# Kernel tuning notes

Hardware: AMD Instinct MI355X
Metric: run time of the kernel (lower is better)

Reference implementation:

```python
import jax, jax.numpy as jnp
import numpy as np

N_NODES = 100000
N_EDGES = 1600000
IN_SIZE = 128
HIDDEN = 128
OUT_SIZE = 64


def setup_inputs() -> dict:
    key = jax.random.key(0)
    k = jax.random.split(key, 8)
    feat = jax.random.normal(k[0], (N_NODES, IN_SIZE), dtype=jnp.float32)
    src = jax.random.randint(k[1], (N_EDGES,), 0, N_NODES, dtype=jnp.int32)
    dst = jax.random.randint(k[2], (N_EDGES,), 0, N_NODES, dtype=jnp.int32)
    # fc_neigh weights for the two SAGEConv layers (stored as [in, out])
    W1 = jax.random.normal(k[3], (IN_SIZE, HIDDEN), dtype=jnp.float32) / np.sqrt(IN_SIZE)
    b1 = jnp.zeros((HIDDEN,), dtype=jnp.float32)
    W2 = jax.random.normal(k[4], (HIDDEN, OUT_SIZE), dtype=jnp.float32) / np.sqrt(HIDDEN)
    b2 = jnp.zeros((OUT_SIZE,), dtype=jnp.float32)
    return {"feat": feat, "W1": W1, "b1": b1, "W2": W2, "b2": b2,
            "src": src, "dst": dst}


def _sage_gcn(h, src, dst, W, b):
    # DGL SAGEConv with aggregator_type='gcn':
    #   neigh = segment_sum over incoming edges of src features
    #   h_neigh = (neigh + h_self) / (in_degree + 1)
    #   out = h_neigh @ W + b   (fc_self is not used for 'gcn')
    neigh = jax.ops.segment_sum(h[src], dst, num_segments=N_NODES)  # [N, d]
    deg = jax.ops.segment_sum(jnp.ones((src.shape[0],), dtype=h.dtype), dst,
                              num_segments=N_NODES)                 # [N]
    h_neigh = (neigh + h) / (deg + 1.0)[:, None]
    return h_neigh @ W + b


def reference(feat, W1, b1, W2, b2, src, dst):
    # dropout(p=0.0) is identity; activation between layers only
    h = _sage_gcn(feat, src, dst, W1, b1)
    h = jax.nn.relu(h)
    h = _sage_gcn(h, src, dst, W2, b2)
    return h
```

## Files before the change

kernel.cpp:

```cpp
#include <hip/hip_runtime.h>

#define NNODES 100000
#define NEDGES 1600000
#define BSHIFT 7
#define NB 782
#define CAP 2560
#define EBLOCKS 391
#define GEMM_BLOCKS 1563

typedef _Float16 f16;
typedef _Float16 v8h __attribute__((ext_vector_type(8)));
typedef float v4f __attribute__((ext_vector_type(4)));

__device__ inline void acc8(float s, uint2 u, float* a) {
    a[0] = fmaf(s, (float)(u.x & 0xFF), a[0]);
    a[1] = fmaf(s, (float)((u.x >> 8) & 0xFF), a[1]);
    a[2] = fmaf(s, (float)((u.x >> 16) & 0xFF), a[2]);
    a[3] = fmaf(s, (float)(u.x >> 24), a[3]);
    a[4] = fmaf(s, (float)(u.y & 0xFF), a[4]);
    a[5] = fmaf(s, (float)((u.y >> 8) & 0xFF), a[5]);
    a[6] = fmaf(s, (float)((u.y >> 16) & 0xFF), a[6]);
    a[7] = fmaf(s, (float)(u.y >> 24), a[7]);
}

__global__ __launch_bounds__(256) void init_k(int* __restrict__ bcur,
                                              const float* __restrict__ W1,
                                              f16* __restrict__ W1t,
                                              const float* __restrict__ W2,
                                              f16* __restrict__ W2t) {
    int t = blockIdx.x * 256 + threadIdx.x;
    if (t < NB) bcur[t] = t * CAP;
    int u = t - 1024;
    if (u >= 0) {
        if (u < 128 * 128) {
            int k = u >> 7, n = u & 127;
            W1t[n * 128 + k] = (f16)W1[k * 128 + n];
        } else if (u < 128 * 128 + 128 * 64) {
            int v = u - 128 * 128;
            int k = v >> 6, n = v & 63;
            W2t[n * 128 + k] = (f16)W2[k * 64 + n];
        }
    }
}

__global__ __launch_bounds__(256) void scatter_gemm1(
    const int* __restrict__ src, const int* __restrict__ dst,
    int* __restrict__ bcur, int* __restrict__ ebuf,
    const float* __restrict__ feat, const f16* __restrict__ W1t,
    unsigned char* __restrict__ z1, float* __restrict__ sc1) {
    constexpr int PITCH = 136;
    __shared__ __align__(16) char smem[128 * PITCH * 2];
    int tid = threadIdx.x;

    if (blockIdx.x < EBLOCKS) {
        int* h = (int*)smem;
        int* base_s = ((int*)smem) + 1024;
        for (int i = tid; i < NB; i += 256) h[i] = 0;
        __syncthreads();
        int base = blockIdx.x * 4096;
        int d[16], sv[16];
        for (int k = 0; k < 16; k++) {
            int e = base + k * 256 + tid;
            if (e < NEDGES) {
                d[k] = dst[e];
                sv[k] = src[e];
                atomicAdd(&h[d[k] >> BSHIFT], 1);
            } else {
                d[k] = -1;
            }
        }
        __syncthreads();
        for (int i = tid; i < NB; i += 256) {
            int c = h[i];
            if (c) base_s[i] = atomicAdd(&bcur[i], c);
            h[i] = 0;
        }
        __syncthreads();
        for (int k = 0; k < 16; k++) {
            if (d[k] >= 0) {
                int b = d[k] >> BSHIFT;
                int slot = atomicAdd(&h[b], 1);
                ebuf[base_s[b] + slot] = sv[k] | ((d[k] & 127) << 24);
            }
        }
        return;
    }

    f16* wlds = (f16*)smem;
    for (int c = tid; c < 128 * 16; c += 256) {
        int n = c >> 4;
        int kc = c & 15;
        *(v8h*)&wlds[n * PITCH + kc * 8] = *(const v8h*)&W1t[n * 128 + kc * 8];
    }
    __syncthreads();

    int wave = tid >> 6, lane = tid & 63, quad = lane >> 4, l16 = lane & 15;
    int m0 = (blockIdx.x - EBLOCKS) * 64 + wave * 16;
    if (m0 >= NNODES) return;

    v8h a[4];
    const float* arow = feat + (long)(m0 + l16) * 128 + quad * 8;
#pragma unroll
    for (int kb = 0; kb < 4; kb++) {
        float4 f0 = *(const float4*)(arow + kb * 32);
        float4 f1 = *(const float4*)(arow + kb * 32 + 4);
        v8h t = {(f16)f0.x, (f16)f0.y, (f16)f0.z, (f16)f0.w,
                 (f16)f1.x, (f16)f1.y, (f16)f1.z, (f16)f1.w};
        a[kb] = t;
    }

    v4f acc[8];
#pragma unroll
    for (int nt = 0; nt < 8; nt++) {
        v4f c4 = {0.f, 0.f, 0.f, 0.f};
        const f16* brow = &wlds[(nt * 16 + l16) * PITCH + quad * 8];
#pragma unroll
        for (int kb = 0; kb < 4; kb++) {
            v8h b = *(const v8h*)(brow + kb * 32);
            c4 = __builtin_amdgcn_mfma_f32_16x16x32_f16(a[kb], b, c4, 0, 0, 0);
        }
        acc[nt] = c4;
    }

#pragma unroll
    for (int r = 0; r < 4; r++) {
        float m = 0.f;
#pragma unroll
        for (int nt = 0; nt < 8; nt++) m = fmaxf(m, fabsf(acc[nt][r]));
        m = fmaxf(m, __shfl_xor(m, 1));
        m = fmaxf(m, __shfl_xor(m, 2));
        m = fmaxf(m, __shfl_xor(m, 4));
        m = fmaxf(m, __shfl_xor(m, 8));
        int row = m0 + quad * 4 + r;
        float rs = (m > 0.f) ? 127.f / m : 0.f;
        if (l16 == 0) sc1[row] = (m > 0.f) ? m / 127.f : 0.f;
#pragma unroll
        for (int nt = 0; nt < 8; nt++) {
            int qv = (int)rintf(acc[nt][r] * rs) + 128;
            z1[(long)row * 128 + nt * 16 + l16] = (unsigned char)qv;
        }
    }
}

__global__ __launch_bounds__(256) void fill_bucket(const int* __restrict__ ebuf,
                                                   const int* __restrict__ bcur,
                                                   int* __restrict__ begs,
                                                   int* __restrict__ ends,
                                                   int* __restrict__ csr) {
    __shared__ int lc[128];
    __shared__ int ls[256];
    int b = blockIdx.x;
    int tid = threadIdx.x;
    if (tid < 128) lc[tid] = 0;
    __syncthreads();
    int ebeg = b * CAP;
    int eend = bcur[b];
    for (int e = ebeg + tid; e < eend; e += 256)
        atomicAdd(&lc[((unsigned)ebuf[e]) >> 24], 1);
    __syncthreads();
    int cnt = (tid < 128) ? lc[tid] : 0;
    ls[tid] = cnt;
    __syncthreads();
    for (int off = 1; off < 256; off <<= 1) {
        int t = (tid >= off) ? ls[tid - off] : 0;
        __syncthreads();
        ls[tid] += t;
        __syncthreads();
    }
    int excl = ls[tid] - cnt;
    int node = (b << BSHIFT) + tid;
    if (tid < 128 && node < NNODES) {
        begs[node] = ebeg + excl;
        ends[node] = ebeg + excl + cnt;
    }
    if (tid < 128) { ls[tid] = excl; lc[tid] = 0; }
    __syncthreads();
    for (int e = ebeg + tid; e < eend; e += 256) {
        int p = ebuf[e];
        int dloc = ((unsigned)p) >> 24;
        int slot = atomicAdd(&lc[dloc], 1);
        csr[ebeg + ls[dloc] + slot] = p & 0xFFFFFF;
    }
}

__global__ __launch_bounds__(1024, 8) void gather128_gemm2(
    const unsigned char* __restrict__ z,
    const float* __restrict__ sc,
    const int* __restrict__ begs, const int* __restrict__ ends,
    const int* __restrict__ csr,
    const float* __restrict__ b1,
    const f16* __restrict__ W2t,
    unsigned char* __restrict__ z2,
    float* __restrict__ sc2)
{
    constexpr int PITCH = 136;
    __shared__ f16 w2lds[64 * PITCH];
    __shared__ f16 atile[64 * PITCH];
    __shared__ int rmax[64];
    int tid = threadIdx.x;

    {
        int n = tid >> 4, kc = tid & 15;
        *(v8h*)&w2lds[n * PITCH + kc * 8] = *(const v8h*)&W2t[n * 128 + kc * 8];
    }
    if (tid < 64) rmax[tid] = 0;

    int wavei = tid >> 6;
    int lane = tid & 63;
    int sub = lane >> 4;
    int c = lane & 15;
    int lnode = wavei * 4 + sub;
    int node = blockIdx.x * 64 + lnode;

    int beg = 0, end = 0;
    if (node < NNODES) { beg = begs[node]; end = ends[node]; }

    unsigned coff = (unsigned)c << 3;

    float a[8];
#pragma unroll
    for (int j = 0; j < 8; j++) a[j] = 0.f;
    float ssum = 0.f;

    if (node < NNODES) {
        float s = sc[node];
        uint2 u = *(const uint2*)(z + (((unsigned)node) << 7) + coff);
        ssum += s;
        acc8(s, u, a);
    }

    int e = beg;
    while (__any(e < end)) {
        float s0 = 0.f, s1 = 0.f, s2 = 0.f, s3 = 0.f;
        float s4 = 0.f, s5 = 0.f, s6 = 0.f, s7 = 0.f;
        uint2 u0 = make_uint2(0, 0), u1 = make_uint2(0, 0);
        uint2 u2 = make_uint2(0, 0), u3 = make_uint2(0, 0);
        uint2 u4 = make_uint2(0, 0), u5 = make_uint2(0, 0);
        uint2 u6 = make_uint2(0, 0), u7 = make_uint2(0, 0);
        if (e     < end) { int i = csr[e    ]; s0 = sc[i]; u0 = *(const uint2*)(z + (((unsigned)i) << 7) + coff); }
        if (e + 1 < end) { int i = csr[e + 1]; s1 = sc[i]; u1 = *(const uint2*)(z + (((unsigned)i) << 7) + coff); }
        if (e + 2 < end) { int i = csr[e + 2]; s2 = sc[i]; u2 = *(const uint2*)(z + (((unsigned)i) << 7) + coff); }
        if (e + 3 < end) { int i = csr[e + 3]; s3 = sc[i]; u3 = *(const uint2*)(z + (((unsigned)i) << 7) + coff); }
        if (e + 4 < end) { int i = csr[e + 4]; s4 = sc[i]; u4 = *(const uint2*)(z + (((unsigned)i) << 7) + coff); }
        if (e + 5 < end) { int i = csr[e + 5]; s5 = sc[i]; u5 = *(const uint2*)(z + (((unsigned)i) << 7) + coff); }
        if (e + 6 < end) { int i = csr[e + 6]; s6 = sc[i]; u6 = *(const uint2*)(z + (((unsigned)i) << 7) + coff); }
        if (e + 7 < end) { int i = csr[e + 7]; s7 = sc[i]; u7 = *(const uint2*)(z + (((unsigned)i) << 7) + coff); }
        ssum += ((s0 + s1) + (s2 + s3)) + ((s4 + s5) + (s6 + s7));
        acc8(s0, u0, a); acc8(s1, u1, a); acc8(s2, u2, a); acc8(s3, u3, a);
        acc8(s4, u4, a); acc8(s5, u5, a); acc8(s6, u6, a); acc8(s7, u7, a);
        e += 8;
    }

    {
        float base = 128.f * ssum;
        float inv = 1.0f / (float)(end - beg + 1);
        float4 bb0 = ((const float4*)b1)[c * 2];
        float4 bb1 = ((const float4*)b1)[c * 2 + 1];
        v8h o = {(f16)fmaxf((a[0] - base) * inv + bb0.x, 0.f),
                 (f16)fmaxf((a[1] - base) * inv + bb0.y, 0.f),
                 (f16)fmaxf((a[2] - base) * inv + bb0.z, 0.f),
                 (f16)fmaxf((a[3] - base) * inv + bb0.w, 0.f),
                 (f16)fmaxf((a[4] - base) * inv + bb1.x, 0.f),
                 (f16)fmaxf((a[5] - base) * inv + bb1.y, 0.f),
                 (f16)fmaxf((a[6] - base) * inv + bb1.z, 0.f),
                 (f16)fmaxf((a[7] - base) * inv + bb1.w, 0.f)};
        *(v8h*)&atile[lnode * PITCH + c * 8] = o;
    }
    __syncthreads();

    {
        int wr = wavei >> 2, wc = wavei & 3;
        int quad = lane >> 4, l16 = lane & 15;
        const f16* arow = &atile[(wr * 16 + l16) * PITCH + quad * 8];
        const f16* brow = &w2lds[(wc * 16 + l16) * PITCH + quad * 8];
        v4f acc = {0.f, 0.f, 0.f, 0.f};
#pragma unroll
        for (int kb = 0; kb < 4; kb++) {
            v8h av = *(const v8h*)(arow + kb * 32);
            v8h bv = *(const v8h*)(brow + kb * 32);
            acc = __builtin_amdgcn_mfma_f32_16x16x32_f16(av, bv, acc, 0, 0, 0);
        }
#pragma unroll
        for (int r = 0; r < 4; r++) {
            float m = fabsf(acc[r]);
            m = fmaxf(m, __shfl_xor(m, 1));
            m = fmaxf(m, __shfl_xor(m, 2));
            m = fmaxf(m, __shfl_xor(m, 4));
            m = fmaxf(m, __shfl_xor(m, 8));
            if (l16 == 0) atomicMax(&rmax[wr * 16 + quad * 4 + r], __float_as_int(m));
        }
        __syncthreads();
#pragma unroll
        for (int r = 0; r < 4; r++) {
            int lrow = wr * 16 + quad * 4 + r;
            int row = blockIdx.x * 64 + lrow;
            if (row < NNODES) {
                float m = __int_as_float(rmax[lrow]);
                float rs = (m > 0.f) ? 127.f / m : 0.f;
                int qv = (int)rintf(acc[r] * rs) + 128;
                z2[(long)row * 64 + wc * 16 + l16] = (unsigned char)qv;
                if (l16 == 0 && wc == 0) sc2[row] = (m > 0.f) ? m / 127.f : 0.f;
            }
        }
    }
}

__global__ __launch_bounds__(256, 8) void gather64(
    const unsigned char* __restrict__ z, const float* __restrict__ sc,
    const int* __restrict__ begs, const int* __restrict__ ends,
    const int* __restrict__ csr,
    const float* __restrict__ bias, float4* __restrict__ out) {
    int tid = threadIdx.x;
    int lane = tid & 63;
    int c = lane & 7;
    int node = blockIdx.x * 32 + (tid >> 3);

    int beg = begs[node];
    int end = ends[node];

    unsigned coff = (unsigned)c << 3;

    float a[8];
#pragma unroll
    for (int j = 0; j < 8; j++) a[j] = 0.f;
    float ssum = 0.f;

    {
        float s = sc[node];
        uint2 u = *(const uint2*)(z + (((unsigned)node) << 6) + coff);
        ssum += s;
        acc8(s, u, a);
    }

    int e = beg;
    while (__any(e < end)) {
        float s0 = 0.f, s1 = 0.f, s2 = 0.f, s3 = 0.f;
        float s4 = 0.f, s5 = 0.f, s6 = 0.f, s7 = 0.f;
        uint2 u0 = make_uint2(0, 0), u1 = make_uint2(0, 0);
        uint2 u2 = make_uint2(0, 0), u3 = make_uint2(0, 0);
        uint2 u4 = make_uint2(0, 0), u5 = make_uint2(0, 0);
        uint2 u6 = make_uint2(0, 0), u7 = make_uint2(0, 0);
        if (e     < end) { int i = csr[e    ]; s0 = sc[i]; u0 = *(const uint2*)(z + (((unsigned)i) << 6) + coff); }
        if (e + 1 < end) { int i = csr[e + 1]; s1 = sc[i]; u1 = *(const uint2*)(z + (((unsigned)i) << 6) + coff); }
        if (e + 2 < end) { int i = csr[e + 2]; s2 = sc[i]; u2 = *(const uint2*)(z + (((unsigned)i) << 6) + coff); }
        if (e + 3 < end) { int i = csr[e + 3]; s3 = sc[i]; u3 = *(const uint2*)(z + (((unsigned)i) << 6) + coff); }
        if (e + 4 < end) { int i = csr[e + 4]; s4 = sc[i]; u4 = *(const uint2*)(z + (((unsigned)i) << 6) + coff); }
        if (e + 5 < end) { int i = csr[e + 5]; s5 = sc[i]; u5 = *(const uint2*)(z + (((unsigned)i) << 6) + coff); }
        if (e + 6 < end) { int i = csr[e + 6]; s6 = sc[i]; u6 = *(const uint2*)(z + (((unsigned)i) << 6) + coff); }
        if (e + 7 < end) { int i = csr[e + 7]; s7 = sc[i]; u7 = *(const uint2*)(z + (((unsigned)i) << 6) + coff); }
        ssum += ((s0 + s1) + (s2 + s3)) + ((s4 + s5) + (s6 + s7));
        acc8(s0, u0, a); acc8(s1, u1, a); acc8(s2, u2, a); acc8(s3, u3, a);
        acc8(s4, u4, a); acc8(s5, u5, a); acc8(s6, u6, a); acc8(s7, u7, a);
        e += 8;
    }

    {
        float base = 128.f * ssum;
        float inv = 1.0f / (float)(end - beg + 1);
        float4 b0 = ((const float4*)bias)[c * 2];
        float4 b1v = ((const float4*)bias)[c * 2 + 1];
        out[(long)node * 16 + c * 2] =
            make_float4((a[0] - base) * inv + b0.x, (a[1] - base) * inv + b0.y,
                        (a[2] - base) * inv + b0.z, (a[3] - base) * inv + b0.w);
        out[(long)node * 16 + c * 2 + 1] =
            make_float4((a[4] - base) * inv + b1v.x, (a[5] - base) * inv + b1v.y,
                        (a[6] - base) * inv + b1v.z, (a[7] - base) * inv + b1v.w);
    }
}

extern "C" void kernel_launch(void* const* d_in, const int* in_sizes, int n_in,
                              void* d_out, int out_size, void* d_ws, size_t ws_size,
                              hipStream_t stream) {
    const float* feat = (const float*)d_in[0];
    const float* W1   = (const float*)d_in[1];
    const float* b1   = (const float*)d_in[2];
    const float* W2   = (const float*)d_in[3];
    const float* b2   = (const float*)d_in[4];
    const int*   src  = (const int*)d_in[5];
    const int*   dst  = (const int*)d_in[6];
    float* out = (float*)d_out;

    char* ws = (char*)d_ws;
    int* bcur = (int*)(ws + 0x0000000);
    int* begs = (int*)(ws + 0x0001000);
    int* ends = (int*)(ws + 0x0063000);
    int* csr  = (int*)(ws + 0x00C5000);
    int* ebuf = (int*)(ws + 0x0870000);
    unsigned char* z1 = (unsigned char*)(ws + 0x1100000);
    float* sc1 = (float*)(ws + 0x2000000);
    unsigned char* z2 = (unsigned char*)(ws + 0x2A00000);
    float* sc2 = (float*)(ws + 0x3100000);
    f16* W1t  = (f16*)(ws + 0x3700000);
    f16* W2t  = (f16*)(ws + 0x3710000);

    init_k<<<100, 256, 0, stream>>>(bcur, W1, W1t, W2, W2t);

    scatter_gemm1<<<EBLOCKS + GEMM_BLOCKS, 256, 0, stream>>>(src, dst, bcur, ebuf,
                                                             feat, W1t, z1, sc1);

    fill_bucket<<<NB, 256, 0, stream>>>(ebuf, bcur, begs, ends, csr);

    gather128_gemm2<<<1563, 1024, 0, stream>>>(z1, sc1, begs, ends, csr, b1, W2t,
                                               z2, sc2);

    gather64<<<3125, 256, 0, stream>>>(z2, sc2, begs, ends, csr, b2, (float4*)out);
}
```

Before: 249.6 us.

## Widen gather loads to 16 bytes and pack neighbor scale into CSR entries

Both gather kernels now have each lane load 16 bytes per neighbor row instead of 8, with fewer lanes per node and more nodes per block. fill_bucket emits a second CSR array holding (src, scale) pairs, so layer 1 reads the scale together with the index and avoids a dependent random load of sc1. Byte-to-float conversion uses the AMD ubyte conversion builtins when they are available. The layer-2 GEMM tile doubles to 128 rows, so each wave handles two MFMA tiles. In exchange there are extra CSR writes, more register pressure, and fewer blocks.

```diff
diff --git a/kernel.cpp b/kernel.cpp
--- a/kernel.cpp
+++ b/kernel.cpp
@@ -12,15 +12,29 @@
 typedef _Float16 v8h __attribute__((ext_vector_type(8)));
 typedef float v4f __attribute__((ext_vector_type(4)));
 
-__device__ inline void acc8(float s, uint2 u, float* a) {
-    a[0] = fmaf(s, (float)(u.x & 0xFF), a[0]);
-    a[1] = fmaf(s, (float)((u.x >> 8) & 0xFF), a[1]);
-    a[2] = fmaf(s, (float)((u.x >> 16) & 0xFF), a[2]);
-    a[3] = fmaf(s, (float)(u.x >> 24), a[3]);
-    a[4] = fmaf(s, (float)(u.y & 0xFF), a[4]);
-    a[5] = fmaf(s, (float)((u.y >> 8) & 0xFF), a[5]);
-    a[6] = fmaf(s, (float)((u.y >> 16) & 0xFF), a[6]);
-    a[7] = fmaf(s, (float)(u.y >> 24), a[7]);
+#if __has_builtin(__builtin_amdgcn_cvt_f32_ubyte0)
+#define CVTB0(u) __builtin_amdgcn_cvt_f32_ubyte0(u)
+#define CVTB1(u) __builtin_amdgcn_cvt_f32_ubyte1(u)
+#define CVTB2(u) __builtin_amdgcn_cvt_f32_ubyte2(u)
+#define CVTB3(u) __builtin_amdgcn_cvt_f32_ubyte3(u)
+#else
+#define CVTB0(u) ((float)((u) & 0xFFu))
+#define CVTB1(u) ((float)(((u) >> 8) & 0xFFu))
+#define CVTB2(u) ((float)(((u) >> 16) & 0xFFu))
+#define CVTB3(u) ((float)((u) >> 24))
+#endif
+
+__device__ inline void accw(float s, unsigned u, float* a) {
+    a[0] = fmaf(s, CVTB0(u), a[0]);
+    a[1] = fmaf(s, CVTB1(u), a[1]);
+    a[2] = fmaf(s, CVTB2(u), a[2]);
+    a[3] = fmaf(s, CVTB3(u), a[3]);
+}
+__device__ inline void acc16(float s, uint4 u, float* a) {
+    accw(s, u.x, a);
+    accw(s, u.y, a + 4);
+    accw(s, u.z, a + 8);
+    accw(s, u.w, a + 12);
 }
 
 __global__ __launch_bounds__(256) void init_k(int* __restrict__ bcur,
@@ -144,9 +158,11 @@
 
 __global__ __launch_bounds__(256) void fill_bucket(const int* __restrict__ ebuf,
                                                    const int* __restrict__ bcur,
+                                                   const float* __restrict__ sc1,
                                                    int* __restrict__ begs,
                                                    int* __restrict__ ends,
-                                                   int* __restrict__ csr) {
+                                                   int* __restrict__ csr4,
+                                                   int2* __restrict__ csr8) {
     __shared__ int lc[128];
     __shared__ int ls[256];
     int b = blockIdx.x;
@@ -178,16 +194,19 @@
     for (int e = ebeg + tid; e < eend; e += 256) {
         int p = ebuf[e];
         int dloc = ((unsigned)p) >> 24;
+        int s = p & 0xFFFFFF;
         int slot = atomicAdd(&lc[dloc], 1);
-        csr[ebeg + ls[dloc] + slot] = p & 0xFFFFFF;
+        int pos = ebeg + ls[dloc] + slot;
+        csr4[pos] = s;
+        csr8[pos] = make_int2(s, __float_as_int(sc1[s]));
     }
 }
 
 __global__ __launch_bounds__(1024, 8) void gather128_gemm2(
     const unsigned char* __restrict__ z,
     const float* __restrict__ sc,
+    const int2* __restrict__ csr8,
     const int* __restrict__ begs, const int* __restrict__ ends,
-    const int* __restrict__ csr,
     const float* __restrict__ b1,
     const f16* __restrict__ W2t,
     unsigned char* __restrict__ z2,
@@ -195,82 +214,106 @@
 {
     constexpr int PITCH = 136;
     __shared__ f16 w2lds[64 * PITCH];
-    __shared__ f16 atile[64 * PITCH];
-    __shared__ int rmax[64];
+    __shared__ f16 atile[128 * PITCH];
+    __shared__ int rmax[128];
     int tid = threadIdx.x;
 
     {
         int n = tid >> 4, kc = tid & 15;
         *(v8h*)&w2lds[n * PITCH + kc * 8] = *(const v8h*)&W2t[n * 128 + kc * 8];
     }
-    if (tid < 64) rmax[tid] = 0;
+    if (tid < 128) rmax[tid] = 0;
 
     int wavei = tid >> 6;
     int lane = tid & 63;
-    int sub = lane >> 4;
-    int c = lane & 15;
-    int lnode = wavei * 4 + sub;
-    int node = blockIdx.x * 64 + lnode;
+    int sub = lane >> 3;
+    int c = lane & 7;
+    int lnode = wavei * 8 + sub;
+    int node = blockIdx.x * 128 + lnode;
 
     int beg = 0, end = 0;
     if (node < NNODES) { beg = begs[node]; end = ends[node]; }
 
-    unsigned coff = (unsigned)c << 3;
-
-    float a[8];
-#pragma unroll
-    for (int j = 0; j < 8; j++) a[j] = 0.f;
+    unsigned coff = (unsigned)c << 4;
+
+    float a[16];
+#pragma unroll
+    for (int j = 0; j < 16; j++) a[j] = 0.f;
     float ssum = 0.f;
 
     if (node < NNODES) {
         float s = sc[node];
-        uint2 u = *(const uint2*)(z + (((unsigned)node) << 7) + coff);
+        uint4 u = *(const uint4*)(z + (((unsigned)node) << 7) + coff);
         ssum += s;
-        acc8(s, u, a);
+        acc16(s, u, a);
     }
 
     int e = beg;
     while (__any(e < end)) {
-        float s0 = 0.f, s1 = 0.f, s2 = 0.f, s3 = 0.f;
-        float s4 = 0.f, s5 = 0.f, s6 = 0.f, s7 = 0.f;
-        uint2 u0 = make_uint2(0, 0), u1 = make_uint2(0, 0);
-        uint2 u2 = make_uint2(0, 0), u3 = make_uint2(0, 0);
-        uint2 u4 = make_uint2(0, 0), u5 = make_uint2(0, 0);
-        uint2 u6 = make_uint2(0, 0), u7 = make_uint2(0, 0);
-        if (e     < end) { int i = csr[e    ]; s0 = sc[i]; u0 = *(const uint2*)(z + (((unsigned)i) << 7) + coff); }
-        if (e + 1 < end) { int i = csr[e + 1]; s1 = sc[i]; u1 = *(const uint2*)(z + (((unsigned)i) << 7) + coff); }
-        if (e + 2 < end) { int i = csr[e + 2]; s2 = sc[i]; u2 = *(const uint2*)(z + (((unsigned)i) << 7) + coff); }
-        if (e + 3 < end) { int i = csr[e + 3]; s3 = sc[i]; u3 = *(const uint2*)(z + (((unsigned)i) << 7) + coff); }
-        if (e + 4 < end) { int i = csr[e + 4]; s4 = sc[i]; u4 = *(const uint2*)(z + (((unsigned)i) << 7) + coff); }
-        if (e + 5 < end) { int i = csr[e + 5]; s5 = sc[i]; u5 = *(const uint2*)(z + (((unsigned)i) << 7) + coff); }
-        if (e + 6 < end) { int i = csr[e + 6]; s6 = sc[i]; u6 = *(const uint2*)(z + (((unsigned)i) << 7) + coff); }
-        if (e + 7 < end) { int i = csr[e + 7]; s7 = sc[i]; u7 = *(const uint2*)(z + (((unsigned)i) << 7) + coff); }
+        int2 q0 = {0, 0}, q1 = {0, 0}, q2 = {0, 0}, q3 = {0, 0};
+        int2 q4 = {0, 0}, q5 = {0, 0}, q6 = {0, 0}, q7 = {0, 0};
+        if (e     < end) q0 = csr8[e];
+        if (e + 1 < end) q1 = csr8[e + 1];
+        if (e + 2 < end) q2 = csr8[e + 2];
+        if (e + 3 < end) q3 = csr8[e + 3];
+        if (e + 4 < end) q4 = csr8[e + 4];
+        if (e + 5 < end) q5 = csr8[e + 5];
+        if (e + 6 < end) q6 = csr8[e + 6];
+        if (e + 7 < end) q7 = csr8[e + 7];
+        uint4 r0 = {0,0,0,0}, r1 = {0,0,0,0}, r2 = {0,0,0,0}, r3 = {0,0,0,0};
+        uint4 r4 = {0,0,0,0}, r5 = {0,0,0,0}, r6 = {0,0,0,0}, r7 = {0,0,0,0};
+        if (e     < end) r0 = *(const uint4*)(z + (((unsigned)q0.x) << 7) + coff);
+        if (e + 1 < end) r1 = *(const uint4*)(z + (((unsigned)q1.x) << 7) + coff);
+        if (e + 2 < end) r2 = *(const uint4*)(z + (((unsigned)q2.x) << 7) + coff);
+        if (e + 3 < end) r3 = *(const uint4*)(z + (((unsigned)q3.x) << 7) + coff);
+        if (e + 4 < end) r4 = *(const uint4*)(z + (((unsigned)q4.x) << 7) + coff);
+        if (e + 5 < end) r5 = *(const uint4*)(z + (((unsigned)q5.x) << 7) + coff);
+        if (e + 6 < end) r6 = *(const uint4*)(z + (((unsigned)q6.x) << 7) + coff);
+        if (e + 7 < end) r7 = *(const uint4*)(z + (((unsigned)q7.x) << 7) + coff);
+        float s0 = __int_as_float(q0.y), s1 = __int_as_float(q1.y);
+        float s2 = __int_as_float(q2.y), s3 = __int_as_float(q3.y);
+        float s4 = __int_as_float(q4.y), s5 = __int_as_float(q5.y);
+        float s6 = __int_as_float(q6.y), s7 = __int_as_float(q7.y);
         ssum += ((s0 + s1) + (s2 + s3)) + ((s4 + s5) + (s6 + s7));
-        acc8(s0, u0, a); acc8(s1, u1, a); acc8(s2, u2, a); acc8(s3, u3, a);
-        acc8(s4, u4, a); acc8(s5, u5, a); acc8(s6, u6, a); acc8(s7, u7, a);
+        acc16(s0, r0, a); acc16(s1, r1, a); acc16(s2, r2, a); acc16(s3, r3, a);
+        acc16(s4, r4, a); acc16(s5, r5, a); acc16(s6, r6, a); acc16(s7, r7, a);
         e += 8;
     }
 
     {
         float base = 128.f * ssum;
         float inv = 1.0f / (float)(end - beg + 1);
-        float4 bb0 = ((const float4*)b1)[c * 2];
-        float4 bb1 = ((const float4*)b1)[c * 2 + 1];
-        v8h o = {(f16)fmaxf((a[0] - base) * inv + bb0.x, 0.f),
-                 (f16)fmaxf((a[1] - base) * inv + bb0.y, 0.f),
-                 (f16)fmaxf((a[2] - base) * inv + bb0.z, 0.f),
-                 (f16)fmaxf((a[3] - base) * inv + bb0.w, 0.f),
-                 (f16)fmaxf((a[4] - base) * inv + bb1.x, 0.f),
-                 (f16)fmaxf((a[5] - base) * inv + bb1.y, 0.f),
-                 (f16)fmaxf((a[6] - base) * inv + bb1.z, 0.f),
-                 (f16)fmaxf((a[7] - base) * inv + bb1.w, 0.f)};
-        *(v8h*)&atile[lnode * PITCH + c * 8] = o;
-    }
-    __syncthreads();
-
-    {
-        int wr = wavei >> 2, wc = wavei & 3;
-        int quad = lane >> 4, l16 = lane & 15;
+        float4 bb0 = ((const float4*)b1)[c * 4];
+        float4 bb1 = ((const float4*)b1)[c * 4 + 1];
+        float4 bb2 = ((const float4*)b1)[c * 4 + 2];
+        float4 bb3 = ((const float4*)b1)[c * 4 + 3];
+        v8h o0 = {(f16)fmaxf((a[0] - base) * inv + bb0.x, 0.f),
+                  (f16)fmaxf((a[1] - base) * inv + bb0.y, 0.f),
+                  (f16)fmaxf((a[2] - base) * inv + bb0.z, 0.f),
+                  (f16)fmaxf((a[3] - base) * inv + bb0.w, 0.f),
+                  (f16)fmaxf((a[4] - base) * inv + bb1.x, 0.f),
+                  (f16)fmaxf((a[5] - base) * inv + bb1.y, 0.f),
+                  (f16)fmaxf((a[6] - base) * inv + bb1.z, 0.f),
+                  (f16)fmaxf((a[7] - base) * inv + bb1.w, 0.f)};
+        v8h o1 = {(f16)fmaxf((a[8] - base) * inv + bb2.x, 0.f),
+                  (f16)fmaxf((a[9] - base) * inv + bb2.y, 0.f),
+                  (f16)fmaxf((a[10] - base) * inv + bb2.z, 0.f),
+                  (f16)fmaxf((a[11] - base) * inv + bb2.w, 0.f),
+                  (f16)fmaxf((a[12] - base) * inv + bb3.x, 0.f),
+                  (f16)fmaxf((a[13] - base) * inv + bb3.y, 0.f),
+                  (f16)fmaxf((a[14] - base) * inv + bb3.z, 0.f),
+                  (f16)fmaxf((a[15] - base) * inv + bb3.w, 0.f)};
+        *(v8h*)&atile[lnode * PITCH + c * 16] = o0;
+        *(v8h*)&atile[lnode * PITCH + c * 16 + 8] = o1;
+    }
+    __syncthreads();
+
+    int quad = lane >> 4, l16 = lane & 15;
+    v4f acc2[2];
+#pragma unroll
+    for (int ti = 0; ti < 2; ti++) {
+        int t = wavei + ti * 16;
+        int wr = t >> 2, wc = t & 3;
         const f16* arow = &atile[(wr * 16 + l16) * PITCH + quad * 8];
         const f16* brow = &w2lds[(wc * 16 + l16) * PITCH + quad * 8];
         v4f acc = {0.f, 0.f, 0.f, 0.f};
@@ -280,6 +323,7 @@
             v8h bv = *(const v8h*)(brow + kb * 32);
             acc = __builtin_amdgcn_mfma_f32_16x16x32_f16(av, bv, acc, 0, 0, 0);
         }
+        acc2[ti] = acc;
 #pragma unroll
         for (int r = 0; r < 4; r++) {
             float m = fabsf(acc[r]);
@@ -289,15 +333,20 @@
             m = fmaxf(m, __shfl_xor(m, 8));
             if (l16 == 0) atomicMax(&rmax[wr * 16 + quad * 4 + r], __float_as_int(m));
         }
-        __syncthreads();
+    }
+    __syncthreads();
+#pragma unroll
+    for (int ti = 0; ti < 2; ti++) {
+        int t = wavei + ti * 16;
+        int wr = t >> 2, wc = t & 3;
 #pragma unroll
         for (int r = 0; r < 4; r++) {
             int lrow = wr * 16 + quad * 4 + r;
-            int row = blockIdx.x * 64 + lrow;
+            int row = blockIdx.x * 128 + lrow;
             if (row < NNODES) {
                 float m = __int_as_float(rmax[lrow]);
                 float rs = (m > 0.f) ? 127.f / m : 0.f;
-                int qv = (int)rintf(acc[r] * rs) + 128;
+                int qv = (int)rintf(acc2[ti][r] * rs) + 128;
                 z2[(long)row * 64 + wc * 16 + l16] = (unsigned char)qv;
                 if (l16 == 0 && wc == 0) sc2[row] = (m > 0.f) ? m / 127.f : 0.f;
             }
@@ -311,60 +360,58 @@
     const int* __restrict__ csr,
     const float* __restrict__ bias, float4* __restrict__ out) {
     int tid = threadIdx.x;
-    int lane = tid & 63;
-    int c = lane & 7;
-    int node = blockIdx.x * 32 + (tid >> 3);
+    int node = blockIdx.x * 64 + (tid >> 2);
+    if (node >= NNODES) return;
+    int c = tid & 3;
+    unsigned coff = (unsigned)c << 4;
 
     int beg = begs[node];
     int end = ends[node];
 
-    unsigned coff = (unsigned)c << 3;
-
-    float a[8];
-#pragma unroll
-    for (int j = 0; j < 8; j++) a[j] = 0.f;
+    float a[16];
+#pragma unroll
+    for (int j = 0; j < 16; j++) a[j] = 0.f;
     float ssum = 0.f;
 
     {
         float s = sc[node];
-        uint2 u = *(const uint2*)(z + (((unsigned)node) << 6) + coff);
+        uint4 u = *(const uint4*)(z + (((unsigned)node) << 6) + coff);
         ssum += s;
-        acc8(s, u, a);
+        acc16(s, u, a);
     }
 
     int e = beg;
     while (__any(e < end)) {
         float s0 = 0.f, s1 = 0.f, s2 = 0.f, s3 = 0.f;
         float s4 = 0.f, s5 = 0.f, s6 = 0.f, s7 = 0.f;
-        uint2 u0 = make_uint2(0, 0), u1 = make_uint2(0, 0);
-        uint2 u2 = make_uint2(0, 0), u3 = make_uint2(0, 0);
-        uint2 u4 = make_uint2(0, 0), u5 = make_uint2(0, 0);
-        uint2 u6 = make_uint2(0, 0), u7 = make_uint2(0, 0);
-        if (e     < end) { int i = csr[e    ]; s0 = sc[i]; u0 = *(const uint2*)(z + (((unsigned)i) << 6) + coff); }
-        if (e + 1 < end) { int i = csr[e + 1]; s1 = sc[i]; u1 = *(const uint2*)(z + (((unsigned)i) << 6) + coff); }
-        if (e + 2 < end) { int i = csr[e + 2]; s2 = sc[i]; u2 = *(const uint2*)(z + (((unsigned)i) << 6) + coff); }
-        if (e + 3 < end) { int i = csr[e + 3]; s3 = sc[i]; u3 = *(const uint2*)(z + (((unsigned)i) << 6) + coff); }
-        if (e + 4 < end) { int i = csr[e + 4]; s4 = sc[i]; u4 = *(const uint2*)(z + (((unsigned)i) << 6) + coff); }
-        if (e + 5 < end) { int i = csr[e + 5]; s5 = sc[i]; u5 = *(const uint2*)(z + (((unsigned)i) << 6) + coff); }
-        if (e + 6 < end) { int i = csr[e + 6]; s6 = sc[i]; u6 = *(const uint2*)(z + (((unsigned)i) << 6) + coff); }
-        if (e + 7 < end) { int i = csr[e + 7]; s7 = sc[i]; u7 = *(const uint2*)(z + (((unsigned)i) << 6) + coff); }
+        uint4 r0 = {0,0,0,0}, r1 = {0,0,0,0}, r2 = {0,0,0,0}, r3 = {0,0,0,0};
+        uint4 r4 = {0,0,0,0}, r5 = {0,0,0,0}, r6 = {0,0,0,0}, r7 = {0,0,0,0};
+        if (e     < end) { int i = csr[e    ]; s0 = sc[i]; r0 = *(const uint4*)(z + (((unsigned)i) << 6) + coff); }
+        if (e + 1 < end) { int i = csr[e + 1]; s1 = sc[i]; r1 = *(const uint4*)(z + (((unsigned)i) << 6) + coff); }
+        if (e + 2 < end) { int i = csr[e + 2]; s2 = sc[i]; r2 = *(const uint4*)(z + (((unsigned)i) << 6) + coff); }
+        if (e + 3 < end) { int i = csr[e + 3]; s3 = sc[i]; r3 = *(const uint4*)(z + (((unsigned)i) << 6) + coff); }
+        if (e + 4 < end) { int i = csr[e + 4]; s4 = sc[i]; r4 = *(const uint4*)(z + (((unsigned)i) << 6) + coff); }
+        if (e + 5 < end) { int i = csr[e + 5]; s5 = sc[i]; r5 = *(const uint4*)(z + (((unsigned)i) << 6) + coff); }
+        if (e + 6 < end) { int i = csr[e + 6]; s6 = sc[i]; r6 = *(const uint4*)(z + (((unsigned)i) << 6) + coff); }
+        if (e + 7 < end) { int i = csr[e + 7]; s7 = sc[i]; r7 = *(const uint4*)(z + (((unsigned)i) << 6) + coff); }
         ssum += ((s0 + s1) + (s2 + s3)) + ((s4 + s5) + (s6 + s7));
-        acc8(s0, u0, a); acc8(s1, u1, a); acc8(s2, u2, a); acc8(s3, u3, a);
-        acc8(s4, u4, a); acc8(s5, u5, a); acc8(s6, u6, a); acc8(s7, u7, a);
+        acc16(s0, r0, a); acc16(s1, r1, a); acc16(s2, r2, a); acc16(s3, r3, a);
+        acc16(s4, r4, a); acc16(s5, r5, a); acc16(s6, r6, a); acc16(s7, r7, a);
         e += 8;
     }
 
     {
         float base = 128.f * ssum;
         float inv = 1.0f / (float)(end - beg + 1);
-        float4 b0 = ((const float4*)bias)[c * 2];
-        float4 b1v = ((const float4*)bias)[c * 2 + 1];
-        out[(long)node * 16 + c * 2] =
-            make_float4((a[0] - base) * inv + b0.x, (a[1] - base) * inv + b0.y,
-                        (a[2] - base) * inv + b0.z, (a[3] - base) * inv + b0.w);
-        out[(long)node * 16 + c * 2 + 1] =
-            make_float4((a[4] - base) * inv + b1v.x, (a[5] - base) * inv + b1v.y,
-                        (a[6] - base) * inv + b1v.z, (a[7] - base) * inv + b1v.w);
+#pragma unroll
+        for (int j = 0; j < 4; j++) {
+            float4 bb = ((const float4*)bias)[c * 4 + j];
+            out[(long)node * 16 + c * 4 + j] =
+                make_float4((a[j * 4 + 0] - base) * inv + bb.x,
+                            (a[j * 4 + 1] - base) * inv + bb.y,
+                            (a[j * 4 + 2] - base) * inv + bb.z,
+                            (a[j * 4 + 3] - base) * inv + bb.w);
+        }
     }
 }
 
@@ -384,12 +431,13 @@
     int* bcur = (int*)(ws + 0x0000000);
     int* begs = (int*)(ws + 0x0001000);
     int* ends = (int*)(ws + 0x0063000);
-    int* csr  = (int*)(ws + 0x00C5000);
+    int* csr4 = (int*)(ws + 0x00C5000);
     int* ebuf = (int*)(ws + 0x0870000);
-    unsigned char* z1 = (unsigned char*)(ws + 0x1100000);
-    float* sc1 = (float*)(ws + 0x2000000);
-    unsigned char* z2 = (unsigned char*)(ws + 0x2A00000);
-    float* sc2 = (float*)(ws + 0x3100000);
+    int2* csr8 = (int2*)(ws + 0x1100000);
+    unsigned char* z1 = (unsigned char*)(ws + 0x2100000);
+    float* sc1 = (float*)(ws + 0x2E00000);
+    unsigned char* z2 = (unsigned char*)(ws + 0x2F00000);
+    float* sc2 = (float*)(ws + 0x3600000);
     f16* W1t  = (f16*)(ws + 0x3700000);
     f16* W2t  = (f16*)(ws + 0x3710000);
 
@@ -398,10 +446,10 @@
     scatter_gemm1<<<EBLOCKS + GEMM_BLOCKS, 256, 0, stream>>>(src, dst, bcur, ebuf,
                                                              feat, W1t, z1, sc1);
 
-    fill_bucket<<<NB, 256, 0, stream>>>(ebuf, bcur, begs, ends, csr);
-
-    gather128_gemm2<<<1563, 1024, 0, stream>>>(z1, sc1, begs, ends, csr, b1, W2t,
-                                               z2, sc2);
-
-    gather64<<<3125, 256, 0, stream>>>(z2, sc2, begs, ends, csr, b2, (float4*)out);
-}
+    fill_bucket<<<NB, 256, 0, stream>>>(ebuf, bcur, sc1, begs, ends, csr4, csr8);
+
+    gather128_gemm2<<<782, 1024, 0, stream>>>(z1, sc1, csr8, begs, ends, b1, W2t,
+                                              z2, sc2);
+
+    gather64<<<1563, 256, 0, stream>>>(z2, sc2, begs, ends, csr4, b2, (float4*)out);
+}
```

Result: slower. 334.5 us (+34.0%).
